# Kernel tuning notes

Measured on AMD Instinct MI355X. Metric: run time of the kernel, lower is better.

## Reference

```python
import jax, jax.numpy as jnp
import numpy as np

C = 256      # dim_in == dim_out (residual add requires it)
H = 96
W = 96
Z = 16       # number of (isWithin, dist) pairs
MAXL = 8


def setup_inputs() -> dict:
    key = jax.random.key(0)
    ks = jax.random.split(key, 8)
    x = jax.random.normal(ks[0], (1, C, H, W), jnp.float32)
    # 1x1 convs without bias == channel matmuls with weight [out_ch, in_ch]
    Wq = jax.random.normal(ks[1], (C, C), jnp.float32) / np.sqrt(C).astype(np.float32)
    Wk = jax.random.normal(ks[2], (C, C), jnp.float32) / np.sqrt(C).astype(np.float32)
    Wv = jax.random.normal(ks[3], (C, C), jnp.float32) / np.sqrt(C).astype(np.float32)
    embd = jax.random.normal(ks[4], (2, 2 * MAXL + 1, C), jnp.float32)  # N(0,1) as in torch
    Wproj = jax.random.normal(ks[5], (C, C + 1), jnp.float32) / np.sqrt(C + 1).astype(np.float32)
    dist = jax.random.randint(ks[6], (Z,), 0, 2 * MAXL + 1) - MAXL      # in [-maxl, maxl]
    isWithin = jax.random.randint(ks[7], (Z,), 0, 2)                     # in {0, 1}
    return {"x": x, "Wq": Wq, "Wk": Wk, "Wv": Wv, "embd": embd,
            "Wproj": Wproj, "dist": dist, "isWithin": isWithin}


def reference(x, Wq, Wk, Wv, embd, Wproj, dist, isWithin):
    b, c, hh, ww = x.shape
    n = hh * ww
    maxl = (embd.shape[1] - 1) // 2
    xf = x.reshape(b, c, n)                                  # [b, c, n]
    q = jnp.einsum('oc,bcn->bon', Wq, xf)                    # 1x1 conv == channel matmul
    k = jnp.einsum('oc,bcn->bon', Wk, xf)
    v = jnp.einsum('oc,bcn->bon', Wv, xf)
    # full (unscaled) attention over spatial tokens, softmax along q axis
    att = jax.nn.softmax(jnp.einsum('bck,bcq->bkq', k, q), axis=-1)  # [b, n, n]
    Y = jnp.einsum('bkq,bck->bcq', att, v)                   # [b, c, n]
    out = Y.reshape(b, c, hh, ww) + x                        # residual
    # relative-distance embedding gather: [z, c]
    rel = embd[isWithin, dist + maxl]
    pos = jnp.einsum('zc,bcn->bzn', rel, xf)                 # [b, z, n] (u=1 folded)
    pos = pos.reshape(b * pos.shape[1], 1, hh, ww)           # [(b z), 1, hh, ww]
    z = pos.shape[0]
    out_rep = jnp.tile(out, (z, 1, 1, 1))                    # [z, c, hh, ww] (b == 1)
    cat = jnp.concatenate([out_rep, pos], axis=1)            # [z, c+1, hh, ww]
    return jnp.einsum('oc,zchw->zohw', Wproj, cat)           # final 1x1 conv
```

## Files before the change

### kernel.cpp

```cpp
#include <hip/hip_runtime.h>
#include <hip/hip_bf16.h>

typedef __bf16 bf8 __attribute__((ext_vector_type(8)));
typedef __bf16 bfx4 __attribute__((ext_vector_type(4)));
typedef float f4 __attribute__((ext_vector_type(4)));

#define NTOK 9216
#define CDIM 256
#define LOG2E 1.44269504f
#define PSHIFT 32.0f

__device__ inline bf8 ldfrag(const __bf16* p, int ld) {
  int l = threadIdx.x & 63;
  return *reinterpret_cast<const bf8*>(p + (l & 15) * ld + ((l >> 4) << 3));
}
__device__ inline f4 mfma16(bf8 a, bf8 b, f4 c) {
  return __builtin_amdgcn_mfma_f32_16x16x32_bf16(a, b, c, 0, 0, 0);
}
__device__ inline void gl2lds(const __bf16* g, __bf16* l) {
  __builtin_amdgcn_global_load_lds(
      (const __attribute__((address_space(1))) void*)g,
      (__attribute__((address_space(3))) void*)l, 16, 0, 0);
}

template <int EPI>
__global__ __launch_bounds__(256) void gemm128(const __bf16* __restrict__ A, int lda,
                                               const __bf16* __restrict__ Bt, int ldb,
                                               void* __restrict__ Cv, int ldc, int K,
                                               const float* __restrict__ aux0,
                                               const float* __restrict__ aux1) {
  __shared__ __bf16 As[128 * 32];
  __shared__ __bf16 Bs[128 * 32];
  const int tid = threadIdx.x;
  const int w = tid >> 6, lane = tid & 63;
  const int lc = lane & 15, quad = lane >> 4;
  const int m0 = blockIdx.x * 128, n0 = blockIdx.y * 128;
  const int wm = (w & 1) << 6, wn = (w >> 1) << 6;
  const int r0 = (w * 2) * 16 + (lane >> 2);
  const int cg = (lane & 3) * 8;
  const __bf16* gA0 = A + (size_t)(m0 + r0) * lda + cg;
  const __bf16* gA1 = A + (size_t)(m0 + r0 + 16) * lda + cg;
  const __bf16* gB0 = Bt + (size_t)(n0 + r0) * ldb + cg;
  const __bf16* gB1 = Bt + (size_t)(n0 + r0 + 16) * ldb + cg;
  __bf16* lA0 = As + (w * 2) * 512;
  __bf16* lA1 = As + (w * 2 + 1) * 512;
  __bf16* lB0 = Bs + (w * 2) * 512;
  __bf16* lB1 = Bs + (w * 2 + 1) * 512;

  f4 acc[4][4] = {};
  for (int kk = 0; kk < K; kk += 32) {
    __syncthreads();
    gl2lds(gA0 + kk, lA0);
    gl2lds(gA1 + kk, lA1);
    gl2lds(gB0 + kk, lB0);
    gl2lds(gB1 + kk, lB1);
    __syncthreads();
    bf8 af[4], bfr[4];
    for (int i = 0; i < 4; i++) af[i] = ldfrag(As + (wm + 16 * i) * 32, 32);
    for (int j = 0; j < 4; j++) bfr[j] = ldfrag(Bs + (wn + 16 * j) * 32, 32);
    for (int i = 0; i < 4; i++)
      for (int j = 0; j < 4; j++) acc[i][j] = mfma16(af[i], bfr[j], acc[i][j]);
  }
  if (EPI == 4) {
    float* outp = (float*)Cv;
    const int z0 = blockIdx.z * 4;
    for (int i = 0; i < 4; i++)
      for (int r = 0; r < 4; r++) {
        int o = m0 + wm + 16 * i + quad * 4 + r;
        float wo = aux1[o];
        for (int j = 0; j < 4; j++) {
          int n = n0 + wn + 16 * j + lc;
          float b = acc[i][j][r];
          for (int z = z0; z < z0 + 4; z++)
            outp[((size_t)z * 256 + o) * NTOK + n] =
                b + wo * aux0[(size_t)z * NTOK + n];
        }
      }
  } else {
    for (int i = 0; i < 4; i++)
      for (int j = 0; j < 4; j++)
        for (int r = 0; r < 4; r++) {
          size_t idx = (size_t)(m0 + wm + 16 * i + quad * 4 + r) * ldc +
                       (n0 + wn + 16 * j + lc);
          ((__bf16*)Cv)[idx] = (__bf16)acc[i][j][r];
        }
  }
}

__global__ __launch_bounds__(256) void sgemm_kernel(const __bf16* __restrict__ Kt,
                                                    const __bf16* __restrict__ Qt,
                                                    __bf16* __restrict__ Pp,
                                                    float* __restrict__ Pd) {
  __shared__ __bf16 As[3][128 * 32];
  __shared__ __bf16 Bs[3][128 * 32];
  const int tid = threadIdx.x;
  const int w = tid >> 6, lane = tid & 63;
  const int lc = lane & 15, quad = lane >> 4;
  const int m0 = blockIdx.x * 128;
  const int n0 = blockIdx.y * 128;
  const int wm = (w & 1) << 6, wn = (w >> 1) << 6;
  const int r0 = w * 32 + (lane >> 2);
  const int cg = (lane & 3) * 8;
  const __bf16* gA0 = Kt + (size_t)(m0 + r0) * 512 + cg;
  const __bf16* gA1 = Kt + (size_t)(m0 + r0 + 16) * 512 + cg;
  const __bf16* gB0 = Qt + (size_t)(n0 + r0) * 512 + cg;
  const __bf16* gB1 = Qt + (size_t)(n0 + r0 + 16) * 512 + cg;
  const int la = w * 1024;

  for (int p = 0; p < 2; p++) {
    gl2lds(gA0 + p * 32, &As[p][la]);
    gl2lds(gA1 + p * 32, &As[p][la + 512]);
    gl2lds(gB0 + p * 32, &Bs[p][la]);
    gl2lds(gB1 + p * 32, &Bs[p][la + 512]);
  }

  f4 acc[4][4] = {};
  int cur = 0;
  for (int s = 0; s < 8; s++) {
    asm volatile("s_waitcnt vmcnt(4)" ::: "memory");
    __builtin_amdgcn_sched_barrier(0);
    __builtin_amdgcn_s_barrier();
    __builtin_amdgcn_sched_barrier(0);
    int sp = (s + 2 < 8) ? s + 2 : 7;
    int nb = cur + 2;
    if (nb >= 3) nb -= 3;
    gl2lds(gA0 + sp * 32, &As[nb][la]);
    gl2lds(gA1 + sp * 32, &As[nb][la + 512]);
    gl2lds(gB0 + sp * 32, &Bs[nb][la]);
    gl2lds(gB1 + sp * 32, &Bs[nb][la + 512]);
    __builtin_amdgcn_sched_barrier(0);
    bf8 af[4], bfr[4];
    for (int i = 0; i < 4; i++) af[i] = ldfrag(&As[cur][(wm + 16 * i) * 32], 32);
    for (int j = 0; j < 4; j++) bfr[j] = ldfrag(&Bs[cur][(wn + 16 * j) * 32], 32);
    for (int i = 0; i < 4; i++)
      for (int j = 0; j < 4; j++) acc[i][j] = mfma16(af[i], bfr[j], acc[i][j]);
    cur = cur + 1;
    if (cur >= 3) cur = 0;
  }

  float dsum[4][4];
  for (int i = 0; i < 4; i++)
    for (int r = 0; r < 4; r++) dsum[i][r] = 0.f;
  for (int j = 0; j < 4; j++) {
    int q = n0 + wn + 16 * j + lc;
    for (int i = 0; i < 4; i++) {
      int ktb = m0 + wm + 16 * i;
      int c2 = ((i & 1) << 1) | (quad >> 1);
      bfx4 pk;
      for (int r = 0; r < 4; r++) {
        float e = exp2f(acc[i][j][r] - PSHIFT);
        dsum[i][r] += e;
        pk[r] = (__bf16)e;
      }
      __bf16* dst = Pp + ((size_t)(ktb >> 5) * NTOK + q) * 32 +
                    ((c2 ^ (lc & 3)) << 3) + ((quad & 1) << 2);
      *reinterpret_cast<bfx4*>(dst) = pk;
    }
  }
  for (int i = 0; i < 4; i++)
    for (int r = 0; r < 4; r++) {
      float d = dsum[i][r];
      d += __shfl_xor(d, 1);
      d += __shfl_xor(d, 2);
      d += __shfl_xor(d, 4);
      d += __shfl_xor(d, 8);
      dsum[i][r] = d;
    }
  if (lc == 0) {
    int mb = blockIdx.y * 2 + (w >> 1);
    for (int i = 0; i < 4; i++)
      for (int r = 0; r < 4; r++) {
        int kt = m0 + wm + 16 * i + quad * 4 + r;
        Pd[(size_t)kt * 144 + mb] = dsum[i][r];
      }
  }
}

__global__ __launch_bounds__(256) void prep_kernel(
    const float* Wq, const float* Wk, const float* Wv, const float* embd,
    const float* Wproj, const int* dist, const int* isWithin,
    __bf16* Wqkb, __bf16* Wvb, __bf16* Wpb, float* wl, __bf16* rel) {
  int tid = blockIdx.x * 256 + threadIdx.x;
  if (tid < 65536) {
    Wqkb[tid] = (__bf16)(Wq[tid] * LOG2E);
    Wqkb[65536 + tid] = (__bf16)Wk[tid];
    Wvb[tid] = (__bf16)Wv[tid];
    int o = tid >> 8, c = tid & 255;
    Wpb[tid] = (__bf16)Wproj[o * 257 + c];
    if (c == 0) wl[o] = Wproj[o * 257 + 256];
  }
  if (tid < 16 * 256) {
    int z = tid >> 8, c = tid & 255;
    rel[tid] = (__bf16)embd[(isWithin[z] * 17 + dist[z] + 8) * 256 + c];
  }
}

__global__ __launch_bounds__(256) void transpose_kernel(const float* x, __bf16* Xt) {
  __shared__ __bf16 tile[32][33];
  int n0 = blockIdx.x * 32;
  int c0 = blockIdx.y * 32;
  int tx = threadIdx.x & 31, ty = threadIdx.x >> 5;
  for (int i = 0; i < 32; i += 8)
    tile[ty + i][tx] = (__bf16)x[(c0 + ty + i) * NTOK + n0 + tx];
  __syncthreads();
  for (int i = 0; i < 32; i += 8)
    Xt[(n0 + ty + i) * CDIM + c0 + tx] = tile[tx][ty + i];
}

__global__ __launch_bounds__(256) void gemm_pos(const __bf16* rel, const __bf16* Xt,
                                                float* pos) {
  int n0 = blockIdx.x * 256 + (threadIdx.x >> 6) * 64;
  f4 acc[4] = {};
  for (int ks = 0; ks < 256; ks += 32) {
    bf8 a = ldfrag(rel + ks, 256);
    for (int j = 0; j < 4; j++) {
      bf8 b = ldfrag(Xt + (n0 + 16 * j) * 256 + ks, 256);
      acc[j] = mfma16(a, b, acc[j]);
    }
  }
  int l = threadIdx.x & 63, lc = l & 15, quad = l >> 4;
  for (int j = 0; j < 4; j++)
    for (int r = 0; r < 4; r++)
      pos[(quad * 4 + r) * NTOK + n0 + 16 * j + lc] = acc[j][r];
}

__global__ __launch_bounds__(256) void combine_stats(const float* __restrict__ Pd,
                                                     float* dinv) {
  int kt = blockIdx.x * 4 + (threadIdx.x >> 6);
  int lane = threadIdx.x & 63;
  const float* pd = Pd + (size_t)kt * 144;
  float d = pd[lane] + pd[lane + 64] + ((lane < 16) ? pd[lane + 128] : 0.f);
  for (int off = 1; off < 64; off <<= 1) d += __shfl_xor(d, off);
  if (lane == 0) dinv[kt] = 1.0f / d;
}

__global__ __launch_bounds__(256) void vscale_kernel(const __bf16* __restrict__ V,
                                                     const float* __restrict__ dinv,
                                                     __bf16* __restrict__ Vs) {
  size_t off = ((size_t)blockIdx.x * 256 + threadIdx.x) * 8;
  bf8 v = *reinterpret_cast<const bf8*>(V + off);
  int c = (int)(off / NTOK);
  int kt = (int)(off % NTOK);
  f4 dl = *reinterpret_cast<const f4*>(dinv + kt);
  f4 dh = *reinterpret_cast<const f4*>(dinv + kt + 4);
  bf8 o;
  for (int j = 0; j < 4; j++) o[j] = (__bf16)((float)v[j] * dl[j]);
  for (int j = 0; j < 4; j++) o[4 + j] = (__bf16)((float)v[4 + j] * dh[j]);
  int c2 = (kt >> 3) & 3;
  size_t dst = (size_t)c * NTOK + (kt & ~31) + (((c2 ^ (c & 3))) << 3);
  *reinterpret_cast<bf8*>(Vs + dst) = o;
}

template <int NSTEP>
__global__ __launch_bounds__(256) void pv_kernel(const __bf16* __restrict__ P,
                                                 const __bf16* __restrict__ Vp,
                                                 float* __restrict__ Ypart) {
  __shared__ __bf16 As[3][64 * 32];
  __shared__ __bf16 Bs[3][256 * 32];
  const int tid = threadIdx.x;
  const int w = tid >> 6, lane = tid & 63;
  const int lc = lane & 15, quad = lane >> 4;
  const int q0 = blockIdx.x * 64;
  const int z = blockIdx.y;
  const int wn = w << 6;
  const int sb0 = z * NSTEP;
  const __bf16* gA = P + ((size_t)sb0 * NTOK + q0) * 32 + w * 512 + lane * 8;
  const size_t aStride = (size_t)NTOK * 32;
  const __bf16* gB = Vp + (size_t)(w * 64 + (lane >> 2)) * NTOK + sb0 * 32 +
                     ((lane & 3) << 3);

  for (int p = 0; p < 2; p++) {
    gl2lds(gA + (size_t)p * aStride, &As[p][w * 512]);
    for (int u = 0; u < 4; u++)
      gl2lds(gB + (size_t)(16 * u) * NTOK + p * 32, &Bs[p][(w * 64 + 16 * u) * 32]);
  }

  f4 acc[4][4] = {};
  int cur = 0;
  const int swz = (quad ^ (lc & 3)) << 3;
  for (int s = 0; s < NSTEP; s++) {
    asm volatile("s_waitcnt vmcnt(5)" ::: "memory");
    __builtin_amdgcn_sched_barrier(0);
    __builtin_amdgcn_s_barrier();
    __builtin_amdgcn_sched_barrier(0);
    int sp = (s + 2 < NSTEP) ? s + 2 : NSTEP - 1;
    int nb = cur + 2;
    if (nb >= 3) nb -= 3;
    gl2lds(gA + (size_t)sp * aStride, &As[nb][w * 512]);
    for (int u = 0; u < 4; u++)
      gl2lds(gB + (size_t)(16 * u) * NTOK + sp * 32, &Bs[nb][(w * 64 + 16 * u) * 32]);
    __builtin_amdgcn_sched_barrier(0);
    bf8 af[4], bfr[4];
    for (int i = 0; i < 4; i++)
      af[i] = *reinterpret_cast<const bf8*>(&As[cur][(16 * i + lc) * 32 + swz]);
    for (int j = 0; j < 4; j++)
      bfr[j] = *reinterpret_cast<const bf8*>(&Bs[cur][(wn + 16 * j + lc) * 32 + swz]);
    for (int i = 0; i < 4; i++)
      for (int j = 0; j < 4; j++) acc[i][j] = mfma16(af[i], bfr[j], acc[i][j]);
    cur = cur + 1;
    if (cur >= 3) cur = 0;
  }

  float* Yp = Ypart + (size_t)z * NTOK * 256;
  for (int i = 0; i < 4; i++)
    for (int j = 0; j < 4; j++)
      for (int r = 0; r < 4; r++)
        Yp[(size_t)(q0 + 16 * i + quad * 4 + r) * 256 + wn + 16 * j + lc] =
            acc[i][j][r];
}

__global__ __launch_bounds__(256) void combine_y_kernel(const float* __restrict__ Ypart,
                                                        const __bf16* __restrict__ Xt,
                                                        __bf16* outT, int zp) {
  int i = blockIdx.x * 256 + threadIdx.x;
  f4 y = {};
  for (int z = 0; z < zp; z++) {
    f4 p = reinterpret_cast<const f4*>(Ypart + (size_t)z * NTOK * 256)[i];
    for (int t = 0; t < 4; t++) y[t] += p[t];
  }
  bfx4 xv = reinterpret_cast<const bfx4*>(Xt)[i];
  bfx4 o;
  for (int t = 0; t < 4; t++) o[t] = (__bf16)(y[t] + (float)xv[t]);
  reinterpret_cast<bfx4*>(outT)[i] = o;
}

extern "C" void kernel_launch(void* const* d_in, const int* in_sizes, int n_in,
                              void* d_out, int out_size, void* d_ws, size_t ws_size,
                              hipStream_t stream) {
  const float* x = (const float*)d_in[0];
  const float* Wq = (const float*)d_in[1];
  const float* Wk = (const float*)d_in[2];
  const float* Wv = (const float*)d_in[3];
  const float* embd = (const float*)d_in[4];
  const float* Wproj = (const float*)d_in[5];
  const int* dist = (const int*)d_in[6];
  const int* isW = (const int*)d_in[7];
  float* out = (float*)d_out;

  char* w8 = (char*)d_ws;
  __bf16* Xt = (__bf16*)(w8 + 0);
  __bf16* QKt = (__bf16*)(w8 + 4718592);
  __bf16* V = (__bf16*)(w8 + 14155776);
  __bf16* Wqkb = (__bf16*)(w8 + 18874368);
  __bf16* Wvb = (__bf16*)(w8 + 19136512);
  __bf16* Wpb = (__bf16*)(w8 + 19267584);
  __bf16* rel = (__bf16*)(w8 + 19398656);
  float* wl = (float*)(w8 + 19406848);
  float* pos = (float*)(w8 + 19407872);
  float* dinv = (float*)(w8 + 20034560);
  __bf16* Vs = (__bf16*)(w8 + 20971520);
  const size_t sOff = 29508608;
  __bf16* P = (__bf16*)(w8 + sOff);
  float* Pd = (float*)(w8 + sOff + 171966464);
  const size_t ypOff = sOff + 171966464 + 5308416;
  float* Ypart = (float*)(w8 + ypOff);
  __bf16* outT = (__bf16*)(w8 + sOff);

  static const int ZPS[] = {6, 4, 3, 2, 1};
  int zp = 1;
  for (int i = 0; i < 5; i++)
    if (ypOff + (size_t)ZPS[i] * 9437184 <= ws_size) { zp = ZPS[i]; break; }

  prep_kernel<<<256, 256, 0, stream>>>(Wq, Wk, Wv, embd, Wproj, dist, isW,
                                       Wqkb, Wvb, Wpb, wl, rel);
  transpose_kernel<<<dim3(288, 8), 256, 0, stream>>>(x, Xt);
  gemm128<1><<<dim3(72, 4), 256, 0, stream>>>(Xt, 256, Wqkb, 256, QKt, 512, 256,
                                              nullptr, nullptr);
  gemm128<1><<<dim3(2, 72), 256, 0, stream>>>(Wvb, 256, Xt, 256, V, NTOK, 256,
                                              nullptr, nullptr);
  gemm_pos<<<36, 256, 0, stream>>>(rel, Xt, pos);
  sgemm_kernel<<<dim3(72, 72), 256, 0, stream>>>(QKt + 256, QKt, P, Pd);
  combine_stats<<<2304, 256, 0, stream>>>(Pd, dinv);
  vscale_kernel<<<1152, 256, 0, stream>>>(V, dinv, Vs);
  switch (zp) {
    case 6: pv_kernel<48><<<dim3(144, 6), 256, 0, stream>>>(P, Vs, Ypart); break;
    case 4: pv_kernel<72><<<dim3(144, 4), 256, 0, stream>>>(P, Vs, Ypart); break;
    case 3: pv_kernel<96><<<dim3(144, 3), 256, 0, stream>>>(P, Vs, Ypart); break;
    case 2: pv_kernel<144><<<dim3(144, 2), 256, 0, stream>>>(P, Vs, Ypart); break;
    default: pv_kernel<288><<<dim3(144, 1), 256, 0, stream>>>(P, Vs, Ypart); break;
  }
  combine_y_kernel<<<2304, 256, 0, stream>>>(Ypart, Xt, outT, zp);
  gemm128<4><<<dim3(2, 72, 4), 256, 0, stream>>>(Wpb, 256, outT, 256, out, NTOK, 256,
                                                 pos, wl);
}
```

Before: 399.6 us.

## Double-buffer score GEMM LDS, raise MFMA priority, widen pos GEMM grid

New measurement: 394.8 us. Within noise of the previous version (-1.2%).

```diff
diff --git a/kernel.cpp b/kernel.cpp
--- a/kernel.cpp
+++ b/kernel.cpp
@@ -91,8 +91,8 @@
                                                     const __bf16* __restrict__ Qt,
                                                     __bf16* __restrict__ Pp,
                                                     float* __restrict__ Pd) {
-  __shared__ __bf16 As[3][128 * 32];
-  __shared__ __bf16 Bs[3][128 * 32];
+  __shared__ __bf16 As[2][128 * 32];
+  __shared__ __bf16 Bs[2][128 * 32];
   const int tid = threadIdx.x;
   const int w = tid >> 6, lane = tid & 63;
   const int lc = lane & 15, quad = lane >> 4;
@@ -115,27 +115,27 @@
   }
 
   f4 acc[4][4] = {};
-  int cur = 0;
   for (int s = 0; s < 8; s++) {
+    const int cur = s & 1;
     asm volatile("s_waitcnt vmcnt(4)" ::: "memory");
     __builtin_amdgcn_sched_barrier(0);
     __builtin_amdgcn_s_barrier();
-    __builtin_amdgcn_sched_barrier(0);
-    int sp = (s + 2 < 8) ? s + 2 : 7;
-    int nb = cur + 2;
-    if (nb >= 3) nb -= 3;
-    gl2lds(gA0 + sp * 32, &As[nb][la]);
-    gl2lds(gA1 + sp * 32, &As[nb][la + 512]);
-    gl2lds(gB0 + sp * 32, &Bs[nb][la]);
-    gl2lds(gB1 + sp * 32, &Bs[nb][la + 512]);
     __builtin_amdgcn_sched_barrier(0);
     bf8 af[4], bfr[4];
     for (int i = 0; i < 4; i++) af[i] = ldfrag(&As[cur][(wm + 16 * i) * 32], 32);
     for (int j = 0; j < 4; j++) bfr[j] = ldfrag(&Bs[cur][(wn + 16 * j) * 32], 32);
+    __builtin_amdgcn_s_setprio(1);
     for (int i = 0; i < 4; i++)
       for (int j = 0; j < 4; j++) acc[i][j] = mfma16(af[i], bfr[j], acc[i][j]);
-    cur = cur + 1;
-    if (cur >= 3) cur = 0;
+    __builtin_amdgcn_s_setprio(0);
+    __builtin_amdgcn_sched_barrier(0);
+    __builtin_amdgcn_s_barrier();
+    __builtin_amdgcn_sched_barrier(0);
+    int sp = (s + 2 < 8) ? s + 2 : 7;
+    gl2lds(gA0 + sp * 32, &As[cur][la]);
+    gl2lds(gA1 + sp * 32, &As[cur][la + 512]);
+    gl2lds(gB0 + sp * 32, &Bs[cur][la]);
+    gl2lds(gB1 + sp * 32, &Bs[cur][la + 512]);
   }
 
   float dsum[4][4];
@@ -209,19 +209,16 @@
 
 __global__ __launch_bounds__(256) void gemm_pos(const __bf16* rel, const __bf16* Xt,
                                                 float* pos) {
-  int n0 = blockIdx.x * 256 + (threadIdx.x >> 6) * 64;
-  f4 acc[4] = {};
+  int n0 = blockIdx.x * 64 + (threadIdx.x >> 6) * 16;
+  f4 acc = {};
   for (int ks = 0; ks < 256; ks += 32) {
     bf8 a = ldfrag(rel + ks, 256);
-    for (int j = 0; j < 4; j++) {
-      bf8 b = ldfrag(Xt + (n0 + 16 * j) * 256 + ks, 256);
-      acc[j] = mfma16(a, b, acc[j]);
-    }
+    bf8 b = ldfrag(Xt + (size_t)n0 * 256 + ks, 256);
+    acc = mfma16(a, b, acc);
   }
   int l = threadIdx.x & 63, lc = l & 15, quad = l >> 4;
-  for (int j = 0; j < 4; j++)
-    for (int r = 0; r < 4; r++)
-      pos[(quad * 4 + r) * NTOK + n0 + 16 * j + lc] = acc[j][r];
+  for (int r = 0; r < 4; r++)
+    pos[(quad * 4 + r) * NTOK + n0 + lc] = acc[r];
 }
 
 __global__ __launch_bounds__(256) void combine_stats(const float* __restrict__ Pd,
@@ -295,8 +292,10 @@
       af[i] = *reinterpret_cast<const bf8*>(&As[cur][(16 * i + lc) * 32 + swz]);
     for (int j = 0; j < 4; j++)
       bfr[j] = *reinterpret_cast<const bf8*>(&Bs[cur][(wn + 16 * j + lc) * 32 + swz]);
+    __builtin_amdgcn_s_setprio(1);
     for (int i = 0; i < 4; i++)
       for (int j = 0; j < 4; j++) acc[i][j] = mfma16(af[i], bfr[j], acc[i][j]);
+    __builtin_amdgcn_s_setprio(0);
     cur = cur + 1;
     if (cur >= 3) cur = 0;
   }
@@ -368,7 +367,7 @@
                                               nullptr, nullptr);
   gemm128<1><<<dim3(2, 72), 256, 0, stream>>>(Wvb, 256, Xt, 256, V, NTOK, 256,
                                               nullptr, nullptr);
-  gemm_pos<<<36, 256, 0, stream>>>(rel, Xt, pos);
+  gemm_pos<<<144, 256, 0, stream>>>(rel, Xt, pos);
   sgemm_kernel<<<dim3(72, 72), 256, 0, stream>>>(QKt + 256, QKt, P, Pd);
   combine_stats<<<2304, 256, 0, stream>>>(Pd, dinv);
   vscale_kernel<<<1152, 256, 0, stream>>>(V, dinv, Vs);
```
